# Optimization experiments

Hardware: AMD Instinct MI355X
Metric: run time of the kernel (lower is better)

The kernel has to match this reference:

```python
import jax, jax.numpy as jnp
import numpy as np

B, Q, PAST = 2, 1024, 1024
T = Q + PAST
HID, NH, NKV, HD = 4096, 32, 8, 128
MAXPOS = 4096
SCALE = HD ** -0.5


def setup_inputs() -> dict:
    key = jax.random.key(0)
    ks = jax.random.split(key, 8)
    hidden_states = jax.random.normal(ks[0], (B, Q, HID), jnp.float32)
    attention_mask = jnp.ones((B, T), jnp.int32)  # all tokens valid
    position_ids = jnp.broadcast_to(
        jnp.arange(PAST, PAST + Q, dtype=jnp.int64)[None, :], (B, Q))
    # standard RoPE caches: [max_pos, head_dim/2]
    inv = 1.0 / (10000.0 ** (np.arange(0, HD, 2, dtype=np.float64) / HD))
    ang = np.arange(MAXPOS, dtype=np.float64)[:, None] * inv[None, :]
    rope_cos_freqs = jnp.asarray(np.cos(ang), jnp.float32)
    rope_sin_freqs = jnp.asarray(np.sin(ang), jnp.float32)
    past_key = jax.random.normal(ks[1], (B, NKV, PAST, HD), jnp.float32)
    past_value = jax.random.normal(ks[2], (B, NKV, PAST, HD), jnp.float32)
    q_w = jax.random.normal(ks[3], (NH * HD, HID), jnp.float32) * 0.02
    k_w = jax.random.normal(ks[4], (NKV * HD, HID), jnp.float32) * 0.02
    v_w = jax.random.normal(ks[5], (NKV * HD, HID), jnp.float32) * 0.02
    o_w = jax.random.normal(ks[6], (HID, NH * HD), jnp.float32) * 0.02
    return {"hidden_states": hidden_states, "attention_mask": attention_mask,
            "position_ids": position_ids, "rope_cos_freqs": rope_cos_freqs,
            "rope_sin_freqs": rope_sin_freqs, "past_key": past_key,
            "past_value": past_value, "q_w": q_w, "k_w": k_w, "v_w": v_w,
            "o_w": o_w}


def _rope(x, cos, sin):
    # x: [B,S,n_heads,HD]; cos/sin: [B,S,HD/2]; non-interleaved (half split)
    d2 = x.shape[-1] // 2
    x1, x2 = x[..., :d2], x[..., d2:]
    c, s = cos[:, :, None, :], sin[:, :, None, :]
    return jnp.concatenate([x1 * c - x2 * s, x2 * c + x1 * s], axis=-1)


def reference(hidden_states, attention_mask, position_ids, rope_cos_freqs,
              rope_sin_freqs, past_key, past_value, q_w, k_w, v_w, o_w):
    b, q_len, _ = hidden_states.shape
    q = jnp.einsum('bsh,oh->bso', hidden_states, q_w).reshape(b, q_len, NH, HD)
    k = jnp.einsum('bsh,oh->bso', hidden_states, k_w).reshape(b, q_len, NKV, HD)
    v = jnp.einsum('bsh,oh->bso', hidden_states, v_w).reshape(b, q_len, NKV, HD)

    cos = rope_cos_freqs[position_ids]  # [B,Q,HD/2]
    sin = rope_sin_freqs[position_ids]
    q = _rope(q, cos, sin)
    k = _rope(k, cos, sin)

    # append to KV cache -> [B,NKV,T,HD]
    present_key = jnp.concatenate([past_key, k.transpose(0, 2, 1, 3)], axis=2)
    present_value = jnp.concatenate([past_value, v.transpose(0, 2, 1, 3)], axis=2)

    # additive causal + padding mask built from cumsum of attention_mask
    all_idx = jnp.cumsum(attention_mask, axis=-1)            # [B,T]
    full = (all_idx[:, -q_len:, None] >= all_idx[:, None, :]) \
        & attention_mask[:, None, :].astype(bool)            # [B,Q,T]
    bias = jnp.where(full, 0.0, -10000.0)[:, None, :, :]     # [B,1,Q,T]

    group = NH // NKV
    k_rep = jnp.repeat(present_key, group, axis=1)           # [B,NH,T,HD]
    v_rep = jnp.repeat(present_value, group, axis=1)

    scores = jnp.einsum('bqhd,bhkd->bhqk', q, k_rep) * SCALE + bias
    probs = jax.nn.softmax(scores, axis=-1)
    ctx = jnp.einsum('bhqk,bhkd->bqhd', probs, v_rep).reshape(b, q_len, NH * HD)
    attn_out = jnp.einsum('bso,ho->bsh', ctx, o_w)
    return attn_out, present_key, present_value
```

## Files before the change

kernel.cpp:

```cpp
#include <hip/hip_runtime.h>
#include <hip/hip_bf16.h>
#include <stdint.h>

typedef __bf16 bf16_t;
typedef bf16_t bf16x8 __attribute__((ext_vector_type(8)));
typedef bf16_t bf16x4 __attribute__((ext_vector_type(4)));
typedef float f32x4 __attribute__((ext_vector_type(4)));

#define B_ 2
#define Q_ 1024
#define PAST_ 1024
#define T_ 2048
#define HID_ 4096
#define NH_ 32
#define NKV_ 8
#define HD_ 128
#define SCALE_ 0.08838834764831845f

__device__ __forceinline__ void async_cp16(const bf16_t* g, bf16_t* l) {
  __builtin_amdgcn_global_load_lds((__attribute__((address_space(1))) void*)g,
                                   (__attribute__((address_space(3))) void*)l, 16, 0, 0);
}

__global__ void cvt_f32_bf16(const float* __restrict__ src, bf16_t* __restrict__ dst, size_t n) {
  size_t i = ((size_t)blockIdx.x * blockDim.x + threadIdx.x) * 8;
  if (i >= n) return;
  float4 a = *(const float4*)(src + i);
  float4 b = *(const float4*)(src + i + 4);
  bf16x8 o;
  o[0] = (bf16_t)a.x; o[1] = (bf16_t)a.y; o[2] = (bf16_t)a.z; o[3] = (bf16_t)a.w;
  o[4] = (bf16_t)b.x; o[5] = (bf16_t)b.y; o[6] = (bf16_t)b.z; o[7] = (bf16_t)b.w;
  *(bf16x8*)(dst + i) = o;
}

__global__ void copy_past(const float* __restrict__ pk, const float* __restrict__ pv,
                          float* __restrict__ oK, float* __restrict__ oV,
                          bf16_t* __restrict__ Kall) {
  size_t i = ((size_t)blockIdx.x * 256 + threadIdx.x) * 4;
  if (i >= (size_t)B_ * NKV_ * PAST_ * HD_) return;
  int d = (int)(i & 127);
  size_t r = i >> 7;
  int t = (int)(r & 1023); r >>= 10;
  int g = (int)(r & 7); int b = (int)(r >> 3);
  size_t dst = (((size_t)b * NKV_ + g) * T_ + t) * HD_ + d;
  float4 k4 = *(const float4*)(pk + i);
  float4 v4 = *(const float4*)(pv + i);
  *(float4*)(oK + dst) = k4;
  *(float4*)(oV + dst) = v4;
  bf16x4 kb; kb[0] = (bf16_t)k4.x; kb[1] = (bf16_t)k4.y; kb[2] = (bf16_t)k4.z; kb[3] = (bf16_t)k4.w;
  *(bf16x4*)(Kall + dst) = kb;
}

__global__ void build_vt(const float* __restrict__ past_v, const float* __restrict__ QKV,
                         bf16_t* __restrict__ Vt) {
  __shared__ bf16_t tile[64][136];
  const int tid = threadIdx.x;
  const int t0 = blockIdx.x * 64, g = blockIdx.y, b = blockIdx.z;
#pragma unroll
  for (int k = 0; k < 8; ++k) {
    int idx = k * 256 + tid;
    int t = idx >> 5, dc = (idx & 31) * 4;
    int tt = t0 + t;
    const float* src = (tt < PAST_)
        ? past_v + ((((size_t)b * NKV_ + g) * PAST_ + tt) * HD_ + dc)
        : QKV + (((size_t)b * Q_ + (tt - PAST_)) * 6144 + 5120 + g * HD_ + dc);
    float4 v4 = *(const float4*)src;
    tile[t][dc] = (bf16_t)v4.x; tile[t][dc + 1] = (bf16_t)v4.y;
    tile[t][dc + 2] = (bf16_t)v4.z; tile[t][dc + 3] = (bf16_t)v4.w;
  }
  __syncthreads();
#pragma unroll
  for (int k = 0; k < 4; ++k) {
    int idx = k * 256 + tid;
    int d = idx >> 3, c = idx & 7;
    bf16x8 o;
#pragma unroll
    for (int j = 0; j < 8; ++j) o[j] = tile[c * 8 + j][d];
    *(bf16x8*)(Vt + ((((size_t)b * NKV_ + g) * HD_ + d) * T_) + t0 + c * 8) = o;
  }
}

__device__ __forceinline__ void stage_tile(const bf16_t* __restrict__ G, int ldg,
                                           bf16_t* __restrict__ L, int tid) {
#pragma unroll
  for (int t = 0; t < 4; ++t) {
    int c = t * 512 + tid;
    int row = c >> 3, sc = (c & 7) ^ (row & 7);
    int cb = t * 512 + (tid & 448);
    async_cp16(G + (size_t)row * ldg + sc * 8, L + (size_t)cb * 8);
  }
}

__device__ __forceinline__ void stage_tileA128(const bf16_t* __restrict__ G, int ldg,
                                               bf16_t* __restrict__ L, int tid) {
#pragma unroll
  for (int t = 0; t < 2; ++t) {
    int c = t * 512 + tid;
    int row = c >> 3, sc = (c & 7) ^ (row & 7);
    int cb = t * 512 + (tid & 448);
    async_cp16(G + (size_t)row * ldg + sc * 8, L + (size_t)cb * 8);
  }
}

__global__ __launch_bounds__(512, 2)
void gemm256(const bf16_t* __restrict__ A, const bf16_t* __restrict__ W,
             float* __restrict__ C, int M, int N, int K) {
  __shared__ bf16_t sm[2][2][16384];
  const int tid = threadIdx.x;
  const int lane = tid & 63;
  const int quad = lane >> 4, l15 = lane & 15;
  const int wave = tid >> 6;
  const int wm = wave >> 2, wn = wave & 3;
  const int bm = blockIdx.y * 256, bn = blockIdx.x * 256;
  const int NT = K >> 6;

  const bf16_t* Ag = A + (size_t)bm * K;
  const bf16_t* Wg = W + (size_t)bn * K;

  f32x4 acc[8][4] = {};

  stage_tile(Ag, K, &sm[0][0][0], tid);
  stage_tile(Wg, K, &sm[0][1][0], tid);
  stage_tile(Ag + 64, K, &sm[1][0][0], tid);
  stage_tile(Wg + 64, K, &sm[1][1][0], tid);
  asm volatile("s_waitcnt vmcnt(8)" ::: "memory");
  __builtin_amdgcn_s_barrier();

  const int arow = wm * 128 + l15;
  const int brow = wn * 64 + l15;
  const int pq = l15 & 7;

  for (int t = 0; t < NT; ++t) {
    const bf16_t* lA = &sm[t & 1][0][0];
    const bf16_t* lB = &sm[t & 1][1][0];
    const int k2 = (t + 2) << 6;
    bf16x8 af[4][2], bf01[2][2], bf23[2][2];

#pragma unroll
    for (int m = 0; m < 4; ++m)
#pragma unroll
      for (int kk = 0; kk < 2; ++kk)
        af[m][kk] = *(const bf16x8*)(lA + (arow + m * 16) * 64 + ((((kk << 2) + quad) ^ pq) << 3));
#pragma unroll
    for (int n = 0; n < 2; ++n)
#pragma unroll
      for (int kk = 0; kk < 2; ++kk)
        bf01[n][kk] = *(const bf16x8*)(lB + (brow + n * 16) * 64 + ((((kk << 2) + quad) ^ pq) << 3));
    __builtin_amdgcn_s_barrier();
    asm volatile("s_waitcnt lgkmcnt(0)" ::: "memory");
    __builtin_amdgcn_sched_barrier(0);
    __builtin_amdgcn_s_setprio(1);
#pragma unroll
    for (int m = 0; m < 4; ++m)
#pragma unroll
      for (int n = 0; n < 2; ++n)
#pragma unroll
        for (int kk = 0; kk < 2; ++kk)
          acc[m][n] = __builtin_amdgcn_mfma_f32_16x16x32_bf16(af[m][kk], bf01[n][kk], acc[m][n], 0, 0, 0);
    __builtin_amdgcn_s_setprio(0);
    __builtin_amdgcn_s_barrier();

#pragma unroll
    for (int n = 0; n < 2; ++n)
#pragma unroll
      for (int kk = 0; kk < 2; ++kk)
        bf23[n][kk] = *(const bf16x8*)(lB + (brow + (n + 2) * 16) * 64 + ((((kk << 2) + quad) ^ pq) << 3));
    __builtin_amdgcn_s_barrier();
    asm volatile("s_waitcnt lgkmcnt(0)" ::: "memory");
    __builtin_amdgcn_sched_barrier(0);
    __builtin_amdgcn_s_setprio(1);
#pragma unroll
    for (int m = 0; m < 4; ++m)
#pragma unroll
      for (int n = 0; n < 2; ++n)
#pragma unroll
        for (int kk = 0; kk < 2; ++kk)
          acc[m][n + 2] = __builtin_amdgcn_mfma_f32_16x16x32_bf16(af[m][kk], bf23[n][kk], acc[m][n + 2], 0, 0, 0);
    __builtin_amdgcn_s_setprio(0);
    __builtin_amdgcn_s_barrier();

#pragma unroll
    for (int m = 0; m < 4; ++m)
#pragma unroll
      for (int kk = 0; kk < 2; ++kk)
        af[m][kk] = *(const bf16x8*)(lA + (arow + (m + 4) * 16) * 64 + ((((kk << 2) + quad) ^ pq) << 3));
    if (t + 2 < NT) stage_tile(Wg + k2, K, &sm[t & 1][1][0], tid);
    __builtin_amdgcn_s_barrier();
    asm volatile("s_waitcnt lgkmcnt(0)" ::: "memory");
    __builtin_amdgcn_sched_barrier(0);
    __builtin_amdgcn_s_setprio(1);
#pragma unroll
    for (int m = 0; m < 4; ++m)
#pragma unroll
      for (int n = 0; n < 2; ++n)
#pragma unroll
        for (int kk = 0; kk < 2; ++kk)
          acc[m + 4][n + 2] = __builtin_amdgcn_mfma_f32_16x16x32_bf16(af[m][kk], bf23[n][kk], acc[m + 4][n + 2], 0, 0, 0);
    __builtin_amdgcn_s_setprio(0);
    __builtin_amdgcn_s_barrier();

    if (t + 2 < NT) stage_tile(Ag + k2, K, &sm[t & 1][0][0], tid);
    __builtin_amdgcn_s_barrier();
    __builtin_amdgcn_s_setprio(1);
#pragma unroll
    for (int m = 0; m < 4; ++m)
#pragma unroll
      for (int n = 0; n < 2; ++n)
#pragma unroll
        for (int kk = 0; kk < 2; ++kk)
          acc[m + 4][n] = __builtin_amdgcn_mfma_f32_16x16x32_bf16(af[m][kk], bf01[n][kk], acc[m + 4][n], 0, 0, 0);
    __builtin_amdgcn_s_setprio(0);
    if (t + 2 < NT)
      asm volatile("s_waitcnt vmcnt(8)" ::: "memory");
    else if (t + 2 == NT)
      asm volatile("s_waitcnt vmcnt(0)" ::: "memory");
    __builtin_amdgcn_s_barrier();
  }

#pragma unroll
  for (int m = 0; m < 8; ++m) {
    int row0 = bm + wm * 128 + m * 16 + quad * 4;
#pragma unroll
    for (int n = 0; n < 4; ++n) {
      int col = bn + wn * 64 + n * 16 + l15;
#pragma unroll
      for (int r = 0; r < 4; ++r)
        C[(size_t)(row0 + r) * N + col] = acc[m][n][r];
    }
  }
}

__global__ __launch_bounds__(512, 2)
void gemm128(const bf16_t* __restrict__ A, const bf16_t* __restrict__ W,
             float* __restrict__ C, int M, int N, int K) {
  __shared__ bf16_t smA[2][8192];
  __shared__ bf16_t smB[2][16384];
  const int tid = threadIdx.x;
  const int lane = tid & 63;
  const int quad = lane >> 4, l15 = lane & 15;
  const int wave = tid >> 6;
  const int wm = wave >> 2, wn = wave & 3;
  const int bm = blockIdx.y * 128, bn = blockIdx.x * 256;
  const int NT = K >> 6;

  const bf16_t* Ag = A + (size_t)bm * K;
  const bf16_t* Wg = W + (size_t)bn * K;

  f32x4 acc[4][4] = {};

  stage_tileA128(Ag, K, &smA[0][0], tid);
  stage_tile(Wg, K, &smB[0][0], tid);
  stage_tileA128(Ag + 64, K, &smA[1][0], tid);
  stage_tile(Wg + 64, K, &smB[1][0], tid);
  asm volatile("s_waitcnt vmcnt(6)" ::: "memory");
  __builtin_amdgcn_s_barrier();

  const int arow = wm * 64 + l15;
  const int brow = wn * 64 + l15;
  const int pq = l15 & 7;

  for (int t = 0; t < NT; ++t) {
    const bf16_t* lA = &smA[t & 1][0];
    const bf16_t* lB = &smB[t & 1][0];
    const int k2 = (t + 2) << 6;
    bf16x8 af[2][2], bf01[2][2], bf23[2][2];

#pragma unroll
    for (int m = 0; m < 2; ++m)
#pragma unroll
      for (int kk = 0; kk < 2; ++kk)
        af[m][kk] = *(const bf16x8*)(lA + (arow + m * 16) * 64 + ((((kk << 2) + quad) ^ pq) << 3));
#pragma unroll
    for (int n = 0; n < 2; ++n)
#pragma unroll
      for (int kk = 0; kk < 2; ++kk)
        bf01[n][kk] = *(const bf16x8*)(lB + (brow + n * 16) * 64 + ((((kk << 2) + quad) ^ pq) << 3));
    __builtin_amdgcn_s_barrier();
    asm volatile("s_waitcnt lgkmcnt(0)" ::: "memory");
    __builtin_amdgcn_sched_barrier(0);
    __builtin_amdgcn_s_setprio(1);
#pragma unroll
    for (int m = 0; m < 2; ++m)
#pragma unroll
      for (int n = 0; n < 2; ++n)
#pragma unroll
        for (int kk = 0; kk < 2; ++kk)
          acc[m][n] = __builtin_amdgcn_mfma_f32_16x16x32_bf16(af[m][kk], bf01[n][kk], acc[m][n], 0, 0, 0);
    __builtin_amdgcn_s_setprio(0);
    __builtin_amdgcn_s_barrier();

#pragma unroll
    for (int n = 0; n < 2; ++n)
#pragma unroll
      for (int kk = 0; kk < 2; ++kk)
        bf23[n][kk] = *(const bf16x8*)(lB + (brow + (n + 2) * 16) * 64 + ((((kk << 2) + quad) ^ pq) << 3));
    __builtin_amdgcn_s_barrier();
    asm volatile("s_waitcnt lgkmcnt(0)" ::: "memory");
    __builtin_amdgcn_sched_barrier(0);
    __builtin_amdgcn_s_setprio(1);
#pragma unroll
    for (int m = 0; m < 2; ++m)
#pragma unroll
      for (int n = 0; n < 2; ++n)
#pragma unroll
        for (int kk = 0; kk < 2; ++kk)
          acc[m][n + 2] = __builtin_amdgcn_mfma_f32_16x16x32_bf16(af[m][kk], bf23[n][kk], acc[m][n + 2], 0, 0, 0);
    __builtin_amdgcn_s_setprio(0);
    __builtin_amdgcn_s_barrier();

#pragma unroll
    for (int m = 0; m < 2; ++m)
#pragma unroll
      for (int kk = 0; kk < 2; ++kk)
        af[m][kk] = *(const bf16x8*)(lA + (arow + (m + 2) * 16) * 64 + ((((kk << 2) + quad) ^ pq) << 3));
    if (t + 2 < NT) stage_tile(Wg + k2, K, &smB[t & 1][0], tid);
    __builtin_amdgcn_s_barrier();
    asm volatile("s_waitcnt lgkmcnt(0)" ::: "memory");
    __builtin_amdgcn_sched_barrier(0);
    __builtin_amdgcn_s_setprio(1);
#pragma unroll
    for (int m = 0; m < 2; ++m)
#pragma unroll
      for (int n = 0; n < 2; ++n)
#pragma unroll
        for (int kk = 0; kk < 2; ++kk)
          acc[m + 2][n + 2] = __builtin_amdgcn_mfma_f32_16x16x32_bf16(af[m][kk], bf23[n][kk], acc[m + 2][n + 2], 0, 0, 0);
    __builtin_amdgcn_s_setprio(0);
    __builtin_amdgcn_s_barrier();

    if (t + 2 < NT) stage_tileA128(Ag + k2, K, &smA[t & 1][0], tid);
    __builtin_amdgcn_s_barrier();
    __builtin_amdgcn_s_setprio(1);
#pragma unroll
    for (int m = 0; m < 2; ++m)
#pragma unroll
      for (int n = 0; n < 2; ++n)
#pragma unroll
        for (int kk = 0; kk < 2; ++kk)
          acc[m + 2][n] = __builtin_amdgcn_mfma_f32_16x16x32_bf16(af[m][kk], bf01[n][kk], acc[m + 2][n], 0, 0, 0);
    __builtin_amdgcn_s_setprio(0);
    if (t + 2 < NT)
      asm volatile("s_waitcnt vmcnt(6)" ::: "memory");
    else if (t + 2 == NT)
      asm volatile("s_waitcnt vmcnt(0)" ::: "memory");
    __builtin_amdgcn_s_barrier();
  }

#pragma unroll
  for (int m = 0; m < 4; ++m) {
    int row0 = bm + wm * 64 + m * 16 + quad * 4;
#pragma unroll
    for (int n = 0; n < 4; ++n) {
      int col = bn + wn * 64 + n * 16 + l15;
#pragma unroll
      for (int r = 0; r < 4; ++r)
        C[(size_t)(row0 + r) * N + col] = acc[m][n][r];
    }
  }
}

__global__ void rope_scatter(const float* __restrict__ QKV, const float* __restrict__ cosf,
                             const float* __restrict__ sinf, const int* __restrict__ pos_ids,
                             bf16_t* __restrict__ Qr, bf16_t* __restrict__ Kall,
                             float* __restrict__ outK, float* __restrict__ outV) {
  int m = blockIdx.x;
  int b = m >> 10, s = m & 1023;
  int pos = pos_ids[(size_t)b * Q_ + s];
  const float* row = QKV + (size_t)m * 6144;
  int tid = threadIdx.x;
  for (int p = tid; p < NH_ * 64; p += 256) {
    int h = p >> 6, d = p & 63;
    float x1 = row[h * 128 + d], x2 = row[h * 128 + d + 64];
    float c = cosf[pos * 64 + d], sn = sinf[pos * 64 + d];
    size_t qb = (((size_t)b * NH_ + h) * Q_ + s) * HD_;
    Qr[qb + d] = (bf16_t)(x1 * c - x2 * sn);
    Qr[qb + d + 64] = (bf16_t)(x2 * c + x1 * sn);
  }
  for (int p = tid; p < NKV_ * 64; p += 256) {
    int g = p >> 6, d = p & 63;
    float x1 = row[4096 + g * 128 + d], x2 = row[4096 + g * 128 + d + 64];
    float c = cosf[pos * 64 + d], sn = sinf[pos * 64 + d];
    float o1 = x1 * c - x2 * sn, o2 = x2 * c + x1 * sn;
    size_t kbi = (((size_t)b * NKV_ + g) * T_ + PAST_ + s) * HD_;
    Kall[kbi + d] = (bf16_t)o1; Kall[kbi + d + 64] = (bf16_t)o2;
    outK[kbi + d] = o1; outK[kbi + d + 64] = o2;
  }
  for (int e = tid; e < NKV_ * HD_; e += 256) {
    int g = e >> 7, d = e & 127;
    float v = row[5120 + g * 128 + d];
    outV[(((size_t)b * NKV_ + g) * T_ + PAST_ + s) * HD_ + d] = v;
  }
}

__global__ __launch_bounds__(256, 2)
void attn_fwd(const bf16_t* __restrict__ Qr, const bf16_t* __restrict__ Kall,
              const bf16_t* __restrict__ Vt, bf16_t* __restrict__ Ctx) {
  __shared__ bf16_t lK[2][64 * 128];
  __shared__ bf16_t lV[2][128 * 64];
  __shared__ bf16_t lP[4 * 16 * 64];
  const int tid = threadIdx.x;
  const int wave = tid >> 6, lane = tid & 63;
  const int quad = lane >> 4, l15 = lane & 15;
  const int i = blockIdx.x;
  const int xcd = i & 7;
  const int j = i >> 3;
  const int pairsel = j & 1;
  const int idx = j >> 1;
  const int h_in = idx & 3;
  const int qt = 15 - (idx >> 2);
  const int b = pairsel, kv = xcd;
  const int h = kv * 4 + h_in;
  const int qbase = qt * 64;
  const int wq = qbase + wave * 16;
  const size_t kvbase = ((size_t)b * NKV_ + kv) * T_ * HD_;
  const size_t vtbase = ((size_t)b * NKV_ + kv) * HD_ * T_;

  auto stageKV = [&](int kb, int s) {
#pragma unroll
    for (int t = 0; t < 4; ++t) {
      int cb = t * 256 + wave * 64;
      int c = cb + lane;
      int row = c >> 4, sc = (c & 15) ^ (row & 15);
      async_cp16(Kall + kvbase + (size_t)(kb + row) * HD_ + sc * 8, lK[s] + (size_t)cb * 8);
    }
#pragma unroll
    for (int t = 0; t < 4; ++t) {
      int cb = t * 256 + wave * 64;
      int c = cb + lane;
      int d = c >> 3, sc = (c & 7) ^ (d & 7);
      async_cp16(Vt + vtbase + (size_t)d * T_ + kb + sc * 8, lV[s] + (size_t)cb * 8);
    }
  };

  bf16x8 qf[4];
  {
    const bf16_t* qg = Qr + ((((size_t)b * NH_ + h) * Q_) + wq + l15) * HD_ + quad * 8;
#pragma unroll
    for (int kk = 0; kk < 4; ++kk) qf[kk] = *(const bf16x8*)(qg + kk * 32);
  }
  f32x4 ctx[8] = {};
  float Mr[4], Lr[4];
#pragma unroll
  for (int r = 0; r < 4; ++r) { Mr[r] = -3.0e30f; Lr[r] = 0.0f; }
  bf16_t* lPw = lP + wave * 16 * 64;
  const int nt = (PAST_ + qbase + 64) >> 6;
  const int wlimit = PAST_ + wq + 15;

  stageKV(0, 0);

  for (int ti = 0; ti < nt; ++ti) {
    const int kb = ti << 6;
    const int cur = ti & 1;
    if (ti + 1 < nt) {
      stageKV(kb + 64, cur ^ 1);
      asm volatile("s_waitcnt vmcnt(8)" ::: "memory");
    } else {
      asm volatile("s_waitcnt vmcnt(0)" ::: "memory");
    }
    __builtin_amdgcn_s_barrier();
    asm volatile("" ::: "memory");
    if (kb <= wlimit) {
      const bf16_t* cK = lK[cur];
      const bf16_t* cV = lV[cur];
      f32x4 sacc[4];
#pragma unroll
      for (int nc = 0; nc < 4; ++nc) sacc[nc] = (f32x4){0.f, 0.f, 0.f, 0.f};
      __builtin_amdgcn_s_setprio(1);
#pragma unroll
      for (int nc = 0; nc < 4; ++nc)
#pragma unroll
        for (int kk = 0; kk < 4; ++kk) {
          bf16x8 bk = *(const bf16x8*)(cK + (nc * 16 + l15) * 128 + (((kk * 4 + quad) ^ l15) << 3));
          sacc[nc] = __builtin_amdgcn_mfma_f32_16x16x32_bf16(qf[kk], bk, sacc[nc], 0, 0, 0);
        }
      __builtin_amdgcn_s_setprio(0);
      bool fullvis = (kb + 63 <= PAST_ + wq);
#pragma unroll
      for (int nc = 0; nc < 4; ++nc) {
        int tkey = kb + nc * 16 + l15;
#pragma unroll
        for (int r = 0; r < 4; ++r) {
          float val = sacc[nc][r] * SCALE_;
          if (!fullvis && tkey > PAST_ + wq + quad * 4 + r) val -= 10000.0f;
          sacc[nc][r] = val;
        }
      }
      float alpha[4], rs[4] = {};
#pragma unroll
      for (int r = 0; r < 4; ++r) {
        float tm = fmaxf(fmaxf(sacc[0][r], sacc[1][r]), fmaxf(sacc[2][r], sacc[3][r]));
#pragma unroll
        for (int mmk = 1; mmk < 16; mmk <<= 1) tm = fmaxf(tm, __shfl_xor(tm, mmk, 64));
        float nm = fmaxf(Mr[r], tm);
        alpha[r] = __expf(Mr[r] - nm);
        Mr[r] = nm;
      }
#pragma unroll
      for (int nc = 0; nc < 4; ++nc)
#pragma unroll
        for (int r = 0; r < 4; ++r) {
          float p = __expf(sacc[nc][r] - Mr[r]);
          rs[r] += p;
          int rho = quad * 4 + r;
          int cslot = ((nc * 2 + (l15 >> 3)) ^ (rho & 7));
          lPw[rho * 64 + cslot * 8 + (l15 & 7)] = (bf16_t)p;
        }
#pragma unroll
      for (int r = 0; r < 4; ++r) {
        float s = rs[r];
#pragma unroll
        for (int mmk = 1; mmk < 16; mmk <<= 1) s += __shfl_xor(s, mmk, 64);
        Lr[r] = Lr[r] * alpha[r] + s;
      }
#pragma unroll
      for (int nc2 = 0; nc2 < 8; ++nc2)
#pragma unroll
        for (int r = 0; r < 4; ++r) ctx[nc2][r] *= alpha[r];
      asm volatile("s_waitcnt lgkmcnt(0)" ::: "memory");
      __builtin_amdgcn_sched_barrier(0);
      __builtin_amdgcn_s_setprio(1);
#pragma unroll
      for (int kk2 = 0; kk2 < 2; ++kk2) {
        bf16x8 ap = *(const bf16x8*)(lPw + l15 * 64 + (((kk2 * 4 + quad) ^ (l15 & 7)) << 3));
#pragma unroll
        for (int nc2 = 0; nc2 < 8; ++nc2) {
          bf16x8 bv = *(const bf16x8*)(cV + (nc2 * 16 + l15) * 64 + (((kk2 * 4 + quad) ^ (l15 & 7)) << 3));
          ctx[nc2] = __builtin_amdgcn_mfma_f32_16x16x32_bf16(ap, bv, ctx[nc2], 0, 0, 0);
        }
      }
      __builtin_amdgcn_s_setprio(0);
    }
    __builtin_amdgcn_sched_barrier(0);
    __builtin_amdgcn_s_barrier();
  }
  float inv[4];
#pragma unroll
  for (int r = 0; r < 4; ++r) inv[r] = 1.0f / Lr[r];
#pragma unroll
  for (int nc2 = 0; nc2 < 8; ++nc2)
#pragma unroll
    for (int r = 0; r < 4; ++r) {
      size_t row = (size_t)b * Q_ + wq + quad * 4 + r;
      Ctx[row * (NH_ * HD_) + h * HD_ + nc2 * 16 + l15] = (bf16_t)(ctx[nc2][r] * inv[r]);
    }
}

extern "C" void kernel_launch(void* const* d_in, const int* in_sizes, int n_in,
                              void* d_out, int out_size, void* d_ws, size_t ws_size,
                              hipStream_t stream) {
  const float* hidden = (const float*)d_in[0];
  const int* pos = (const int*)d_in[2];
  const float* cosf = (const float*)d_in[3];
  const float* sinf = (const float*)d_in[4];
  const float* past_k = (const float*)d_in[5];
  const float* past_v = (const float*)d_in[6];
  const float* q_w = (const float*)d_in[7];
  const float* k_w = (const float*)d_in[8];
  const float* v_w = (const float*)d_in[9];
  const float* o_w = (const float*)d_in[10];

  float* attn_out = (float*)d_out;
  float* outK = attn_out + (size_t)B_ * Q_ * HID_;
  float* outV = outK + (size_t)B_ * NKV_ * T_ * HD_;

  if (ws_size < 150994944) return;
  char* ws = (char*)d_ws;
  bf16_t* Wqkv = (bf16_t*)(ws);
  bf16_t* Xb   = (bf16_t*)(ws + 50331648);
  float*  QKV  = (float*)(ws + 67108864);
  bf16_t* Qr   = (bf16_t*)(ws + 117440512);
  bf16_t* Kall = (bf16_t*)(ws + 134217728);
  bf16_t* Vt   = (bf16_t*)(ws + 142606336);
  bf16_t* Wo   = (bf16_t*)(ws + 67108864);
  bf16_t* Ctx  = (bf16_t*)(ws + 50331648);

  cvt_f32_bf16<<<4096, 256, 0, stream>>>(hidden, Xb, 8388608);
  cvt_f32_bf16<<<8192, 256, 0, stream>>>(q_w, Wqkv, 16777216);
  cvt_f32_bf16<<<2048, 256, 0, stream>>>(k_w, Wqkv + 16777216, 4194304);
  cvt_f32_bf16<<<2048, 256, 0, stream>>>(v_w, Wqkv + 20971520, 4194304);
  copy_past<<<2048, 256, 0, stream>>>(past_k, past_v, outK, outV, Kall);
  gemm256<<<dim3(24, 8), 512, 0, stream>>>(Xb, Wqkv, QKV, 2048, 6144, 4096);
  rope_scatter<<<2048, 256, 0, stream>>>(QKV, cosf, sinf, pos, Qr, Kall, outK, outV);
  build_vt<<<dim3(32, 8, 2), 256, 0, stream>>>(past_v, QKV, Vt);
  cvt_f32_bf16<<<8192, 256, 0, stream>>>(o_w, Wo, 16777216);
  attn_fwd<<<1024, 256, 0, stream>>>(Qr, Kall, Vt, Ctx);
  gemm128<<<dim3(16, 16), 512, 0, stream>>>(Ctx, Wo, attn_out, 2048, 4096, 4096);
}
```

Before: 581.2 us.

## Enlarge attention query tile to 128 rows, fold scale into Q, lazy rescale

```diff
diff --git a/kernel.cpp b/kernel.cpp
--- a/kernel.cpp
+++ b/kernel.cpp
@@ -373,8 +373,8 @@
     float x1 = row[h * 128 + d], x2 = row[h * 128 + d + 64];
     float c = cosf[pos * 64 + d], sn = sinf[pos * 64 + d];
     size_t qb = (((size_t)b * NH_ + h) * Q_ + s) * HD_;
-    Qr[qb + d] = (bf16_t)(x1 * c - x2 * sn);
-    Qr[qb + d + 64] = (bf16_t)(x2 * c + x1 * sn);
+    Qr[qb + d] = (bf16_t)((x1 * c - x2 * sn) * SCALE_);
+    Qr[qb + d + 64] = (bf16_t)((x2 * c + x1 * sn) * SCALE_);
   }
   for (int p = tid; p < NKV_ * 64; p += 256) {
     int g = p >> 6, d = p & 63;
@@ -392,12 +392,12 @@
   }
 }
 
-__global__ __launch_bounds__(256, 2)
+__global__ __launch_bounds__(512, 2)
 void attn_fwd(const bf16_t* __restrict__ Qr, const bf16_t* __restrict__ Kall,
               const bf16_t* __restrict__ Vt, bf16_t* __restrict__ Ctx) {
   __shared__ bf16_t lK[2][64 * 128];
   __shared__ bf16_t lV[2][128 * 64];
-  __shared__ bf16_t lP[4 * 16 * 64];
+  __shared__ bf16_t lP[8 * 16 * 64];
   const int tid = threadIdx.x;
   const int wave = tid >> 6, lane = tid & 63;
   const int quad = lane >> 4, l15 = lane & 15;
@@ -407,27 +407,27 @@
   const int pairsel = j & 1;
   const int idx = j >> 1;
   const int h_in = idx & 3;
-  const int qt = 15 - (idx >> 2);
+  const int qt = 7 - (idx >> 2);
   const int b = pairsel, kv = xcd;
   const int h = kv * 4 + h_in;
-  const int qbase = qt * 64;
+  const int qbase = qt * 128;
   const int wq = qbase + wave * 16;
   const size_t kvbase = ((size_t)b * NKV_ + kv) * T_ * HD_;
   const size_t vtbase = ((size_t)b * NKV_ + kv) * HD_ * T_;
 
   auto stageKV = [&](int kb, int s) {
 #pragma unroll
-    for (int t = 0; t < 4; ++t) {
-      int cb = t * 256 + wave * 64;
-      int c = cb + lane;
+    for (int t = 0; t < 2; ++t) {
+      int c = t * 512 + tid;
       int row = c >> 4, sc = (c & 15) ^ (row & 15);
+      int cb = t * 512 + (tid & 448);
       async_cp16(Kall + kvbase + (size_t)(kb + row) * HD_ + sc * 8, lK[s] + (size_t)cb * 8);
     }
 #pragma unroll
-    for (int t = 0; t < 4; ++t) {
-      int cb = t * 256 + wave * 64;
-      int c = cb + lane;
+    for (int t = 0; t < 2; ++t) {
+      int c = t * 512 + tid;
       int d = c >> 3, sc = (c & 7) ^ (d & 7);
+      int cb = t * 512 + (tid & 448);
       async_cp16(Vt + vtbase + (size_t)d * T_ + kb + sc * 8, lV[s] + (size_t)cb * 8);
     }
   };
@@ -443,7 +443,7 @@
 #pragma unroll
   for (int r = 0; r < 4; ++r) { Mr[r] = -3.0e30f; Lr[r] = 0.0f; }
   bf16_t* lPw = lP + wave * 16 * 64;
-  const int nt = (PAST_ + qbase + 64) >> 6;
+  const int nt = (PAST_ + qbase + 128) >> 6;
   const int wlimit = PAST_ + wq + 15;
 
   stageKV(0, 0);
@@ -453,7 +453,7 @@
     const int cur = ti & 1;
     if (ti + 1 < nt) {
       stageKV(kb + 64, cur ^ 1);
-      asm volatile("s_waitcnt vmcnt(8)" ::: "memory");
+      asm volatile("s_waitcnt vmcnt(4)" ::: "memory");
     } else {
       asm volatile("s_waitcnt vmcnt(0)" ::: "memory");
     }
@@ -475,26 +475,37 @@
         }
       __builtin_amdgcn_s_setprio(0);
       bool fullvis = (kb + 63 <= PAST_ + wq);
-#pragma unroll
-      for (int nc = 0; nc < 4; ++nc) {
-        int tkey = kb + nc * 16 + l15;
-#pragma unroll
-        for (int r = 0; r < 4; ++r) {
-          float val = sacc[nc][r] * SCALE_;
-          if (!fullvis && tkey > PAST_ + wq + quad * 4 + r) val -= 10000.0f;
-          sacc[nc][r] = val;
+      if (!fullvis) {
+#pragma unroll
+        for (int nc = 0; nc < 4; ++nc) {
+          int tkey = kb + nc * 16 + l15;
+#pragma unroll
+          for (int r = 0; r < 4; ++r)
+            if (tkey > PAST_ + wq + quad * 4 + r) sacc[nc][r] -= 10000.0f;
         }
       }
-      float alpha[4], rs[4] = {};
+      float tmax[4];
+      bool need = false;
 #pragma unroll
       for (int r = 0; r < 4; ++r) {
         float tm = fmaxf(fmaxf(sacc[0][r], sacc[1][r]), fmaxf(sacc[2][r], sacc[3][r]));
 #pragma unroll
         for (int mmk = 1; mmk < 16; mmk <<= 1) tm = fmaxf(tm, __shfl_xor(tm, mmk, 64));
-        float nm = fmaxf(Mr[r], tm);
-        alpha[r] = __expf(Mr[r] - nm);
-        Mr[r] = nm;
+        tmax[r] = tm;
+        need = need || (tm > Mr[r] + 8.0f);
       }
+      if (__any(need)) {
+#pragma unroll
+        for (int r = 0; r < 4; ++r) {
+          float nm = fmaxf(Mr[r], tmax[r]);
+          float al = __expf(Mr[r] - nm);
+          Mr[r] = nm;
+          Lr[r] *= al;
+#pragma unroll
+          for (int nc2 = 0; nc2 < 8; ++nc2) ctx[nc2][r] *= al;
+        }
+      }
+      float rs[4] = {};
 #pragma unroll
       for (int nc = 0; nc < 4; ++nc)
 #pragma unroll
@@ -510,12 +521,8 @@
         float s = rs[r];
 #pragma unroll
         for (int mmk = 1; mmk < 16; mmk <<= 1) s += __shfl_xor(s, mmk, 64);
-        Lr[r] = Lr[r] * alpha[r] + s;
+        Lr[r] += s;
       }
-#pragma unroll
-      for (int nc2 = 0; nc2 < 8; ++nc2)
-#pragma unroll
-        for (int r = 0; r < 4; ++r) ctx[nc2][r] *= alpha[r];
       asm volatile("s_waitcnt lgkmcnt(0)" ::: "memory");
       __builtin_amdgcn_sched_barrier(0);
       __builtin_amdgcn_s_setprio(1);
@@ -583,6 +590,6 @@
   rope_scatter<<<2048, 256, 0, stream>>>(QKV, cosf, sinf, pos, Qr, Kall, outK, outV);
   build_vt<<<dim3(32, 8, 2), 256, 0, stream>>>(past_v, QKV, Vt);
   cvt_f32_bf16<<<8192, 256, 0, stream>>>(o_w, Wo, 16777216);
-  attn_fwd<<<1024, 256, 0, stream>>>(Qr, Kall, Vt, Ctx);
+  attn_fwd<<<512, 512, 0, stream>>>(Qr, Kall, Vt, Ctx);
   gemm128<<<dim3(16, 16), 512, 0, stream>>>(Ctx, Wo, attn_out, 2048, 4096, 4096);
 }
```

After: 580.7 us. No clear change (-0.1%).
